# Kernel tuning notes

Hardware: AMD Instinct MI355X
Metric: run time of the kernel (lower is better)

The kernel has to match this reference:

```python
import jax, jax.numpy as jnp
import numpy as np

DIM = 128
CODEBOOK_SIZE = 1024

def setup_inputs() -> dict:
    key = jax.random.key(0)
    k1, k2 = jax.random.split(key)
    x = jax.random.normal(k1, (16, 4096, DIM), dtype=jnp.float32)
    embed = jax.random.normal(k2, (CODEBOOK_SIZE, DIM), dtype=jnp.float32)
    return {"x": x, "embed": embed}

def reference(x, embed):
    # preprocess: flatten leading dims -> (N, d)
    shape = x.shape
    flat = x.reshape(-1, shape[-1])  # (N, d)
    x_sq = jnp.sum(flat * flat, axis=1, keepdims=True)        # (N, 1)
    e_sq = jnp.sum(embed * embed, axis=1)[None, :]            # (1, K)
    dist = -(x_sq - 2.0 * (flat @ embed.T) + e_sq)            # (N, K)
    embed_ind = jnp.argmax(dist, axis=-1)                     # (N,)
    embed_ind = embed_ind.reshape(shape[:-1])                 # (...,)
    quantize = jnp.take(embed, embed_ind, axis=0)             # (..., d)
    return (quantize, embed_ind)
```

## Files before the change

kernel.cpp:

```cpp
#include <hip/hip_runtime.h>

#define NRD   65536
#define DIMD  128
#define KCB   1024
#define RPB   64
#define NBLK  (NRD / RPB)
#define MARGIN 0.18f

typedef float f32x4 __attribute__((ext_vector_type(4)));
typedef short short8 __attribute__((ext_vector_type(8)));

#define WS_ESQ   0
#define WS_CNT   4096
#define WS_LIST  8192
#define WS_B     270336
#define WS_ET2   532480
#define WS_NEED  1056768

__device__ inline unsigned short f2bf(float f) {
    unsigned u = __float_as_uint(f);
    u += 0x7FFFu + ((u >> 16) & 1u);
    return (unsigned short)(u >> 16);
}
__device__ inline float bf2f(unsigned short h) { return __uint_as_float(((unsigned)h) << 16); }

__device__ inline short8 pack_h(float4 a, float4 b) {
    short8 r;
    r[0]=(short)f2bf(a.x); r[1]=(short)f2bf(a.y); r[2]=(short)f2bf(a.z); r[3]=(short)f2bf(a.w);
    r[4]=(short)f2bf(b.x); r[5]=(short)f2bf(b.y); r[6]=(short)f2bf(b.z); r[7]=(short)f2bf(b.w);
    return r;
}
__device__ inline short lo1(float f) { return (short)f2bf(f - bf2f(f2bf(f))); }
__device__ inline short8 pack_l(float4 a, float4 b) {
    short8 r;
    r[0]=lo1(a.x); r[1]=lo1(a.y); r[2]=lo1(a.z); r[3]=lo1(a.w);
    r[4]=lo1(b.x); r[5]=lo1(b.y); r[6]=lo1(b.z); r[7]=lo1(b.w);
    return r;
}

__global__ __launch_bounds__(256, 2) void prep_kernel(const float* __restrict__ embed,
                                                      float* __restrict__ esq,
                                                      float4* __restrict__ bblob,
                                                      float4* __restrict__ et4,
                                                      int* __restrict__ cnt,
                                                      int doTrans) {
    __shared__ float tile[64][129];
    const int t = threadIdx.x;
    {
        int gw   = blockIdx.x * 4 + (t >> 6);
        int lane = t & 63;
        const float* row = embed + (size_t)gw * DIMD;
        float a = row[lane], b = row[lane + 64];
        float v = a * a + b * b;
        #pragma unroll
        for (int off = 32; off >= 1; off >>= 1) v += __shfl_xor(v, off, 64);
        if (lane == 0) esq[gw] = v;
    }
    if (blockIdx.x < 64) {
        int tid  = blockIdx.x * 256 + t;
        int lane = tid & 63;
        int ctg  = (tid >> 6) & 15;
        int ksh  = (tid >> 10) & 1;
        int s    = tid >> 11;
        int chunk = s >> 1, kh = s & 1;
        int ks = kh * 2 + ksh;
        int l15 = lane & 15, l4 = lane >> 4;
        int code = chunk * 256 + ctg * 16 + l15;
        int d0   = ks * 32 + l4 * 8;
        const float4* e4 = (const float4*)(embed + (size_t)code * DIMD + d0);
        short8 v = pack_h(e4[0], e4[1]);
        bblob[tid] = *(float4*)&v;
    }
    if (doTrans && blockIdx.x >= 64 && blockIdx.x < 80) {
        const int c0 = (blockIdx.x - 64) * 64;
        #pragma unroll
        for (int i = 0; i < 8; ++i) {
            int u = t + i * 256;
            int row = u >> 5, col4 = u & 31;
            float4 v = ((const float4*)embed)[(size_t)(c0 + row) * 32 + col4];
            tile[row][col4 * 4 + 0] = v.x;
            tile[row][col4 * 4 + 1] = v.y;
            tile[row][col4 * 4 + 2] = v.z;
            tile[row][col4 * 4 + 3] = v.w;
        }
        __syncthreads();
        #pragma unroll
        for (int i = 0; i < 8; ++i) {
            int u = t + i * 256;
            int d = u >> 4, off = u & 15;
            float4 v;
            v.x = tile[off * 4 + 0][d];
            v.y = tile[off * 4 + 1][d];
            v.z = tile[off * 4 + 2][d];
            v.w = tile[off * 4 + 3][d];
            et4[(size_t)d * 256 + (c0 >> 2) + off] = v;
        }
    }
    if (blockIdx.x == 128 && t == 0) cnt[0] = 0;
}

__global__ __launch_bounds__(512, 4) void vq_mfma(const float* __restrict__ x,
                                                  const float* __restrict__ embed,
                                                  const float* __restrict__ esq,
                                                  const float4* __restrict__ bblob,
                                                  float* __restrict__ out_q,
                                                  float* __restrict__ out_idx,
                                                  int* __restrict__ cnt,
                                                  int* __restrict__ list) {
    __shared__ __align__(16) short Atrans[4][4][512];
    __shared__ __align__(16) short Bb[32][512];
    __shared__ float rbest[4][RPB];
    __shared__ int   rmeta[4][RPB];
    __shared__ float rb2[4][RPB];

    const int t    = threadIdx.x;
    const int lane = t & 63;
    const int w    = __builtin_amdgcn_readfirstlane(t >> 6);
    const int rg   = w >> 2, cg = w & 3;
    const int l15  = lane & 15, l4 = lane >> 4;
    const int row0 = blockIdx.x * RPB;

    const int ksA = w & 3, jh = w >> 2;
    const float4* xs = (const float4*)(x + (size_t)(row0 + lane) * DIMD + ksA * 32 + jh * 16);
    float4 xv0 = xs[0], xv1 = xs[1], xv2 = xs[2], xv3 = xs[3];

#define GLDS(sv) do {                                                                                   \
    const char* g_ = (const char*)bblob + (size_t)(sv) * 32768 + ((size_t)w * 64 + lane) * 16;          \
    _Pragma("unroll")                                                                                   \
    for (int k_ = 0; k_ < 4; ++k_)                                                                      \
        __builtin_amdgcn_global_load_lds(                                                               \
            (const __attribute__((address_space(1))) unsigned int*)(g_ + k_ * 8192),                    \
            (__attribute__((address_space(3))) unsigned int*)&Bb[k_ * 8 + w][0], 16, 0, 0);             \
} while (0)

    GLDS(0);

    const int rtA = lane >> 4, riA = lane & 15;
    *(short8*)&Atrans[ksA][rtA][((jh * 2 + 0) * 16 + riA) * 8] = pack_h(xv0, xv1);
    *(short8*)&Atrans[ksA][rtA][((jh * 2 + 1) * 16 + riA) * 8] = pack_h(xv2, xv3);
    asm volatile("s_waitcnt lgkmcnt(0)" ::: "memory");
    __builtin_amdgcn_s_barrier();

    short8 ahr[4][2];
    #pragma unroll
    for (int ks = 0; ks < 4; ++ks)
        #pragma unroll
        for (int rt = 0; rt < 2; ++rt)
            ahr[ks][rt] = *(const short8*)&Atrans[ks][rg * 2 + rt][lane * 8];
    asm volatile("s_waitcnt lgkmcnt(0)" ::: "memory");
    __builtin_amdgcn_s_barrier();

    *(short8*)&Atrans[ksA][rtA][((jh * 2 + 0) * 16 + riA) * 8] = pack_l(xv0, xv1);
    *(short8*)&Atrans[ksA][rtA][((jh * 2 + 1) * 16 + riA) * 8] = pack_l(xv2, xv3);
    asm volatile("s_waitcnt vmcnt(0) lgkmcnt(0)" ::: "memory");
    __builtin_amdgcn_s_barrier();

    f32x4 acc[2][4];
    float best[2][4]; int bidx[2][4]; float b2[2][4];
    #pragma unroll
    for (int i = 0; i < 2; ++i)
        #pragma unroll
        for (int j = 0; j < 4; ++j) { best[i][j] = -1e30f; bidx[i][j] = 0; b2[i][j] = -1e30f; }

    const float* esqp = esq + cg * 64 + l15;
    float eq0 = 0.f, eq1 = 0.f, eq2 = 0.f, eq3 = 0.f;

#define STEP(khv) do {                                                                  \
    const int s_ = c * 2 + khv;                                                         \
    if (khv == 0) {                                                                     \
        eq0 = esqp[c * 256];      eq1 = esqp[c * 256 + 16];                             \
        eq2 = esqp[c * 256 + 32]; eq3 = esqp[c * 256 + 48];                             \
        _Pragma("unroll")                                                               \
        for (int i_ = 0; i_ < 2; ++i_)                                                  \
            _Pragma("unroll")                                                           \
            for (int j_ = 0; j_ < 4; ++j_) acc[i_][j_] = (f32x4){0.f, 0.f, 0.f, 0.f};   \
    }                                                                                   \
    short8 al_[2][2], bh_[2][4];                                                        \
    _Pragma("unroll")                                                                   \
    for (int ksh_ = 0; ksh_ < 2; ++ksh_) {                                              \
        _Pragma("unroll")                                                               \
        for (int rt_ = 0; rt_ < 2; ++rt_)                                               \
            al_[ksh_][rt_] = *(const short8*)&Atrans[khv * 2 + ksh_][rg * 2 + rt_][lane * 8]; \
        _Pragma("unroll")                                                               \
        for (int ct_ = 0; ct_ < 4; ++ct_)                                               \
            bh_[ksh_][ct_] = *(const short8*)&Bb[ksh_ * 16 + cg * 4 + ct_][lane * 8];   \
    }                                                                                   \
    asm volatile("s_waitcnt lgkmcnt(0)" ::: "memory");                                  \
    __builtin_amdgcn_s_barrier();                            \
    if (s_ < 7) GLDS(s_ + 1);                                   \
    _Pragma("unroll")                                                                   \
    for (int ksh_ = 0; ksh_ < 2; ++ksh_) {                                              \
        _Pragma("unroll")                                                               \
        for (int ct_ = 0; ct_ < 4; ++ct_) {                                             \
            _Pragma("unroll")                                                           \
            for (int rt_ = 0; rt_ < 2; ++rt_) {                                         \
                acc[rt_][ct_] = __builtin_amdgcn_mfma_f32_16x16x32_bf16(ahr[khv * 2 + ksh_][rt_], bh_[ksh_][ct_], acc[rt_][ct_], 0, 0, 0); \
                acc[rt_][ct_] = __builtin_amdgcn_mfma_f32_16x16x32_bf16(al_[ksh_][rt_],           bh_[ksh_][ct_], acc[rt_][ct_], 0, 0, 0); \
            }                                                                           \
        }                                                                               \
    }                                                                                   \
    if (khv == 1) {                           \
        _Pragma("unroll")                                                               \
        for (int ct_ = 0; ct_ < 4; ++ct_) {                                             \
            int code_ = c * 256 + cg * 64 + ct_ * 16 + l15;                             \
            float eq_ = (ct_ == 0) ? eq0 : (ct_ == 1) ? eq1 : (ct_ == 2) ? eq2 : eq3;   \
            _Pragma("unroll")                                                           \
            for (int rt_ = 0; rt_ < 2; ++rt_)                                           \
                _Pragma("unroll")                                                       \
                for (int r_ = 0; r_ < 4; ++r_) {                                        \
                    float sc_ = 2.0f * acc[rt_][ct_][r_] - eq_;                         \
                    b2[rt_][r_] = fmaxf(b2[rt_][r_], fminf(sc_, best[rt_][r_]));        \
                    if (sc_ > best[rt_][r_]) { best[rt_][r_] = sc_; bidx[rt_][r_] = code_; } \
                }                                                                       \
        }                                                                               \
    }                                                                                   \
    if (s_ < 7) {                                                                       \
        asm volatile("s_waitcnt vmcnt(0)" ::: "memory");          \
        __builtin_amdgcn_s_barrier();                                                   \
    }                                                                                   \
} while (0)

    for (int c = 0; c < 4; ++c) {
        STEP(0); STEP(1);
    }
#undef STEP
#undef GLDS

    #pragma unroll
    for (int rt = 0; rt < 2; ++rt)
        #pragma unroll
        for (int r = 0; r < 4; ++r) {
            float v = best[rt][r]; int i = bidx[rt][r]; float s2 = b2[rt][r];
            #pragma unroll
            for (int off = 1; off < 16; off <<= 1) {
                float ov = __shfl_xor(v, off, 64);
                int   oi = __shfl_xor(i, off, 64);
                float o2 = __shfl_xor(s2, off, 64);
                s2 = fmaxf(fmaxf(s2, o2), fminf(v, ov));
                bool sw = (ov > v) || (ov == v && oi < i);
                if (sw) { v = ov; i = oi; }
            }
            if (l15 == 0) {
                int rl = rg * 32 + rt * 16 + l4 * 4 + r;
                rbest[cg][rl] = v;
                rmeta[cg][rl] = i;
                rb2[cg][rl]   = s2;
            }
        }
    __syncthreads();
    if (t < RPB) {
        float b = rbest[0][t]; int i = rmeta[0][t]; float s2 = rb2[0][t];
        #pragma unroll
        for (int g = 1; g < 4; ++g) {
            float ob = rbest[g][t]; int oi = rmeta[g][t]; float o2 = rb2[g][t];
            s2 = fmaxf(fmaxf(s2, o2), fminf(b, ob));
            bool sw = (ob > b) || (ob == b && oi < i);
            if (sw) { b = ob; i = oi; }
        }
        out_idx[row0 + t] = (float)i;
        if (s2 >= b - MARGIN) { int pos = atomicAdd(cnt, 1); list[pos] = row0 + t; }
        rmeta[0][t] = i;
    }
    __syncthreads();
    {
        int row = t >> 3, part = t & 7;
        int idx = rmeta[0][row];
        const float4* src = (const float4*)(embed + (size_t)idx * DIMD + part * 16);
        float4* dst = (float4*)(out_q + (size_t)(row0 + row) * DIMD + part * 16);
        #pragma unroll
        for (int q = 0; q < 4; ++q) dst[q] = src[q];
    }
}

__global__ __launch_bounds__(256, 2) void trans_kernel(const float* __restrict__ embed,
                                                       float4* __restrict__ et4) {
    __shared__ float tile[64][129];
    const int t = threadIdx.x;
    const int c0 = blockIdx.x * 64;
    #pragma unroll
    for (int i = 0; i < 8; ++i) {
        int u = t + i * 256;
        int row = u >> 5, col4 = u & 31;
        float4 v = ((const float4*)embed)[(size_t)(c0 + row) * 32 + col4];
        tile[row][col4 * 4 + 0] = v.x;
        tile[row][col4 * 4 + 1] = v.y;
        tile[row][col4 * 4 + 2] = v.z;
        tile[row][col4 * 4 + 3] = v.w;
    }
    __syncthreads();
    #pragma unroll
    for (int i = 0; i < 8; ++i) {
        int u = t + i * 256;
        int d = u >> 4, off = u & 15;
        float4 v;
        v.x = tile[off * 4 + 0][d];
        v.y = tile[off * 4 + 1][d];
        v.z = tile[off * 4 + 2][d];
        v.w = tile[off * 4 + 3][d];
        et4[(size_t)d * 256 + (c0 >> 2) + off] = v;
    }
}

__global__ __launch_bounds__(256, 2) void refine_kernel(const float* __restrict__ x,
                                                        const float* __restrict__ embed,
                                                        const float* __restrict__ esq,
                                                        const f32x4* __restrict__ et4,
                                                        float* __restrict__ out_q,
                                                        float* __restrict__ out_idx,
                                                        const int* __restrict__ cnt,
                                                        const int* __restrict__ list) {
    __shared__ float xls[4][4][128];
    const int t = threadIdx.x, lane = t & 63, w = t >> 6;
    const int n = cnt[0];
    const int njobs = (n + 3) >> 2;
    for (int job = blockIdx.x * 4 + w; job < njobs; job += gridDim.x * 4) {
        int rows[4];
        #pragma unroll
        for (int i = 0; i < 4; ++i) {
            int li = job * 4 + i; if (li >= n) li = n - 1;
            rows[i] = list[li];
        }
        float xsq[4];
        #pragma unroll
        for (int i = 0; i < 4; ++i) {
            float2 xv = *(const float2*)(x + (size_t)rows[i] * DIMD + lane * 2);
            xls[w][i][lane * 2]     = xv.x;
            xls[w][i][lane * 2 + 1] = xv.y;
            float s = xv.x * xv.x + xv.y * xv.y;
            #pragma unroll
            for (int off = 32; off >= 1; off >>= 1) s += __shfl_xor(s, off, 64);
            xsq[i] = s;
        }
        f32x4 acc[4][4];
        #pragma unroll
        for (int i = 0; i < 4; ++i)
            #pragma unroll
            for (int g = 0; g < 4; ++g) acc[i][g] = (f32x4){0.f, 0.f, 0.f, 0.f};

        for (int d0 = 0; d0 < 32; ++d0) {
            float4 xd[4];
            #pragma unroll
            for (int i = 0; i < 4; ++i) xd[i] = *(const float4*)&xls[w][i][d0 * 4];
            #pragma unroll
            for (int dd = 0; dd < 4; ++dd) {
                const f32x4* ep = et4 + (size_t)(d0 * 4 + dd) * 256 + lane;
                f32x4 e0 = ep[0], e1 = ep[64], e2 = ep[128], e3 = ep[192];
                #pragma unroll
                for (int i = 0; i < 4; ++i) {
                    float xsc = (dd == 0) ? xd[i].x : (dd == 1) ? xd[i].y
                              : (dd == 2) ? xd[i].z : xd[i].w;
                    acc[i][0] = e0 * xsc + acc[i][0];
                    acc[i][1] = e1 * xsc + acc[i][1];
                    acc[i][2] = e2 * xsc + acc[i][2];
                    acc[i][3] = e3 * xsc + acc[i][3];
                }
            }
        }

        #pragma unroll
        for (int i = 0; i < 4; ++i) {
            float bv = -1e30f; int bi = 0;
            #pragma unroll
            for (int g = 0; g < 4; ++g) {
                float4 eq = *(const float4*)&esq[g * 256 + lane * 4];
                #pragma unroll
                for (int c2 = 0; c2 < 4; ++c2) {
                    float eqv = (c2 == 0) ? eq.x : (c2 == 1) ? eq.y : (c2 == 2) ? eq.z : eq.w;
                    float sc = -(__fadd_rn(__fsub_rn(xsq[i], __fmul_rn(2.0f, acc[i][g][c2])), eqv));
                    int code = g * 256 + lane * 4 + c2;
                    if (sc > bv) { bv = sc; bi = code; }
                }
            }
            #pragma unroll
            for (int off = 32; off >= 1; off >>= 1) {
                float ov = __shfl_xor(bv, off, 64);
                int   oi = __shfl_xor(bi, off, 64);
                if (ov > bv || (ov == bv && oi < bi)) { bv = ov; bi = oi; }
            }
            if (lane == 0) out_idx[rows[i]] = (float)bi;
            if (lane < 32) {
                float4 v = ((const float4*)embed)[(size_t)bi * 32 + lane];
                ((float4*)out_q)[(size_t)rows[i] * 32 + lane] = v;
            }
        }
    }
}

extern "C" void kernel_launch(void* const* d_in, const int* in_sizes, int n_in,
                              void* d_out, int out_size, void* d_ws, size_t ws_size,
                              hipStream_t stream) {
    const float* x     = (const float*)d_in[0];
    const float* embed = (const float*)d_in[1];
    float* out     = (float*)d_out;
    float* out_q   = out;
    float* out_idx = out + (size_t)NRD * DIMD;

    char*  wsb  = (char*)d_ws;
    float* esq  = (float*)(wsb + WS_ESQ);
    int*   cnt  = (int*)(wsb + WS_CNT);
    int*   list = (int*)(wsb + WS_LIST);
    float4* bblob = (float4*)(wsb + WS_B);

    const int fused = (ws_size >= (size_t)WS_NEED) ? 1 : 0;
    f32x4* et4 = fused ? (f32x4*)(wsb + WS_ET2) : (f32x4*)(wsb + WS_B);

    prep_kernel  <<<dim3(256),  dim3(256), 0, stream>>>(embed, esq, bblob, (float4*)et4, cnt, fused);
    vq_mfma      <<<dim3(NBLK), dim3(512), 0, stream>>>(x, embed, esq, bblob, out_q, out_idx, cnt, list);
    if (!fused)
        trans_kernel<<<dim3(16), dim3(256), 0, stream>>>(embed, (float4*)et4);
    refine_kernel<<<dim3(256),  dim3(256), 0, stream>>>(x, embed, esq, et4, out_q, out_idx, cnt, list);
}
```

Before: 89.36 us.

## Drop bf16 low-part split for x and pipeline codebook loads in half-stages

Removes the hi/lo bf16 split of x, which halves the MFMA count per step. To keep argmax correct it widens the refinement margin from 0.18 to 0.40, so more rows fall into the exact fp32 fallback path. It also aliases the A staging buffer onto the B buffer, caches codebook norms in LDS, and restructures the B loads into half-stage prefetches with vmcnt-based waits. The risks are more rows needing refinement and more barriers per stage.

```diff
diff --git a/kernel.cpp b/kernel.cpp
--- a/kernel.cpp
+++ b/kernel.cpp
@@ -5,7 +5,7 @@
 #define KCB   1024
 #define RPB   64
 #define NBLK  (NRD / RPB)
-#define MARGIN 0.18f
+#define MARGIN 0.40f
 
 typedef float f32x4 __attribute__((ext_vector_type(4)));
 typedef short short8 __attribute__((ext_vector_type(8)));
@@ -22,19 +22,11 @@
     u += 0x7FFFu + ((u >> 16) & 1u);
     return (unsigned short)(u >> 16);
 }
-__device__ inline float bf2f(unsigned short h) { return __uint_as_float(((unsigned)h) << 16); }
 
 __device__ inline short8 pack_h(float4 a, float4 b) {
     short8 r;
     r[0]=(short)f2bf(a.x); r[1]=(short)f2bf(a.y); r[2]=(short)f2bf(a.z); r[3]=(short)f2bf(a.w);
     r[4]=(short)f2bf(b.x); r[5]=(short)f2bf(b.y); r[6]=(short)f2bf(b.z); r[7]=(short)f2bf(b.w);
-    return r;
-}
-__device__ inline short lo1(float f) { return (short)f2bf(f - bf2f(f2bf(f))); }
-__device__ inline short8 pack_l(float4 a, float4 b) {
-    short8 r;
-    r[0]=lo1(a.x); r[1]=lo1(a.y); r[2]=lo1(a.z); r[3]=lo1(a.w);
-    r[4]=lo1(b.x); r[5]=lo1(b.y); r[6]=lo1(b.z); r[7]=lo1(b.w);
     return r;
 }
 
@@ -107,8 +99,8 @@
                                                   float* __restrict__ out_idx,
                                                   int* __restrict__ cnt,
                                                   int* __restrict__ list) {
-    __shared__ __align__(16) short Atrans[4][4][512];
     __shared__ __align__(16) short Bb[32][512];
+    __shared__ float esqs[KCB];
     __shared__ float rbest[4][RPB];
     __shared__ int   rmeta[4][RPB];
     __shared__ float rb2[4][RPB];
@@ -120,24 +112,17 @@
     const int l15  = lane & 15, l4 = lane >> 4;
     const int row0 = blockIdx.x * RPB;
 
+    const float2 ev = *(const float2*)(esq + t * 2);
+
     const int ksA = w & 3, jh = w >> 2;
     const float4* xs = (const float4*)(x + (size_t)(row0 + lane) * DIMD + ksA * 32 + jh * 16);
     float4 xv0 = xs[0], xv1 = xs[1], xv2 = xs[2], xv3 = xs[3];
 
-#define GLDS(sv) do {                                                                                   \
-    const char* g_ = (const char*)bblob + (size_t)(sv) * 32768 + ((size_t)w * 64 + lane) * 16;          \
-    _Pragma("unroll")                                                                                   \
-    for (int k_ = 0; k_ < 4; ++k_)                                                                      \
-        __builtin_amdgcn_global_load_lds(                                                               \
-            (const __attribute__((address_space(1))) unsigned int*)(g_ + k_ * 8192),                    \
-            (__attribute__((address_space(3))) unsigned int*)&Bb[k_ * 8 + w][0], 16, 0, 0);             \
-} while (0)
-
-    GLDS(0);
-
+    short (*Atrans)[4][512] = (short (*)[4][512])&Bb[0][0];
     const int rtA = lane >> 4, riA = lane & 15;
     *(short8*)&Atrans[ksA][rtA][((jh * 2 + 0) * 16 + riA) * 8] = pack_h(xv0, xv1);
     *(short8*)&Atrans[ksA][rtA][((jh * 2 + 1) * 16 + riA) * 8] = pack_h(xv2, xv3);
+    *(float2*)&esqs[t * 2] = ev;
     asm volatile("s_waitcnt lgkmcnt(0)" ::: "memory");
     __builtin_amdgcn_s_barrier();
 
@@ -150,10 +135,19 @@
     asm volatile("s_waitcnt lgkmcnt(0)" ::: "memory");
     __builtin_amdgcn_s_barrier();
 
-    *(short8*)&Atrans[ksA][rtA][((jh * 2 + 0) * 16 + riA) * 8] = pack_l(xv0, xv1);
-    *(short8*)&Atrans[ksA][rtA][((jh * 2 + 1) * 16 + riA) * 8] = pack_l(xv2, xv3);
-    asm volatile("s_waitcnt vmcnt(0) lgkmcnt(0)" ::: "memory");
-    __builtin_amdgcn_s_barrier();
+#define GLDS_HALF(s2, kshv) do {                                                                        \
+    const char* g_ = (const char*)bblob + (size_t)(s2) * 32768 + (size_t)(kshv) * 16384                 \
+                   + ((size_t)w * 64 + lane) * 16;                                                      \
+    __builtin_amdgcn_global_load_lds(                                                                   \
+        (const __attribute__((address_space(1))) unsigned int*)(g_),                                    \
+        (__attribute__((address_space(3))) unsigned int*)&Bb[(kshv) * 16 + w][0], 16, 0, 0);            \
+    __builtin_amdgcn_global_load_lds(                                                                   \
+        (const __attribute__((address_space(1))) unsigned int*)(g_ + 8192),                             \
+        (__attribute__((address_space(3))) unsigned int*)&Bb[(kshv) * 16 + 8 + w][0], 16, 0, 0);        \
+} while (0)
+
+    GLDS_HALF(0, 0);
+    GLDS_HALF(0, 1);
 
     f32x4 acc[2][4];
     float best[2][4]; int bidx[2][4]; float b2[2][4];
@@ -162,69 +156,63 @@
         #pragma unroll
         for (int j = 0; j < 4; ++j) { best[i][j] = -1e30f; bidx[i][j] = 0; b2[i][j] = -1e30f; }
 
-    const float* esqp = esq + cg * 64 + l15;
     float eq0 = 0.f, eq1 = 0.f, eq2 = 0.f, eq3 = 0.f;
 
-#define STEP(khv) do {                                                                  \
-    const int s_ = c * 2 + khv;                                                         \
-    if (khv == 0) {                                                                     \
-        eq0 = esqp[c * 256];      eq1 = esqp[c * 256 + 16];                             \
-        eq2 = esqp[c * 256 + 32]; eq3 = esqp[c * 256 + 48];                             \
-        _Pragma("unroll")                                                               \
-        for (int i_ = 0; i_ < 2; ++i_)                                                  \
-            _Pragma("unroll")                                                           \
-            for (int j_ = 0; j_ < 4; ++j_) acc[i_][j_] = (f32x4){0.f, 0.f, 0.f, 0.f};   \
-    }                                                                                   \
-    short8 al_[2][2], bh_[2][4];                                                        \
-    _Pragma("unroll")                                                                   \
-    for (int ksh_ = 0; ksh_ < 2; ++ksh_) {                                              \
-        _Pragma("unroll")                                                               \
-        for (int rt_ = 0; rt_ < 2; ++rt_)                                               \
-            al_[ksh_][rt_] = *(const short8*)&Atrans[khv * 2 + ksh_][rg * 2 + rt_][lane * 8]; \
-        _Pragma("unroll")                                                               \
-        for (int ct_ = 0; ct_ < 4; ++ct_)                                               \
-            bh_[ksh_][ct_] = *(const short8*)&Bb[ksh_ * 16 + cg * 4 + ct_][lane * 8];   \
-    }                                                                                   \
-    asm volatile("s_waitcnt lgkmcnt(0)" ::: "memory");                                  \
-    __builtin_amdgcn_s_barrier();                            \
-    if (s_ < 7) GLDS(s_ + 1);                                   \
-    _Pragma("unroll")                                                                   \
-    for (int ksh_ = 0; ksh_ < 2; ++ksh_) {                                              \
-        _Pragma("unroll")                                                               \
-        for (int ct_ = 0; ct_ < 4; ++ct_) {                                             \
-            _Pragma("unroll")                                                           \
-            for (int rt_ = 0; rt_ < 2; ++rt_) {                                         \
-                acc[rt_][ct_] = __builtin_amdgcn_mfma_f32_16x16x32_bf16(ahr[khv * 2 + ksh_][rt_], bh_[ksh_][ct_], acc[rt_][ct_], 0, 0, 0); \
-                acc[rt_][ct_] = __builtin_amdgcn_mfma_f32_16x16x32_bf16(al_[ksh_][rt_],           bh_[ksh_][ct_], acc[rt_][ct_], 0, 0, 0); \
-            }                                                                           \
-        }                                                                               \
-    }                                                                                   \
-    if (khv == 1) {                           \
-        _Pragma("unroll")                                                               \
-        for (int ct_ = 0; ct_ < 4; ++ct_) {                                             \
-            int code_ = c * 256 + cg * 64 + ct_ * 16 + l15;                             \
-            float eq_ = (ct_ == 0) ? eq0 : (ct_ == 1) ? eq1 : (ct_ == 2) ? eq2 : eq3;   \
-            _Pragma("unroll")                                                           \
-            for (int rt_ = 0; rt_ < 2; ++rt_)                                           \
-                _Pragma("unroll")                                                       \
-                for (int r_ = 0; r_ < 4; ++r_) {                                        \
-                    float sc_ = 2.0f * acc[rt_][ct_][r_] - eq_;                         \
-                    b2[rt_][r_] = fmaxf(b2[rt_][r_], fminf(sc_, best[rt_][r_]));        \
-                    if (sc_ > best[rt_][r_]) { best[rt_][r_] = sc_; bidx[rt_][r_] = code_; } \
-                }                                                                       \
-        }                                                                               \
-    }                                                                                   \
-    if (s_ < 7) {                                                                       \
-        asm volatile("s_waitcnt vmcnt(0)" ::: "memory");          \
-        __builtin_amdgcn_s_barrier();                                                   \
-    }                                                                                   \
-} while (0)
-
+    #pragma unroll
     for (int c = 0; c < 4; ++c) {
-        STEP(0); STEP(1);
-    }
-#undef STEP
-#undef GLDS
+      #pragma unroll
+      for (int khv = 0; khv < 2; ++khv) {
+        #pragma unroll
+        for (int ksh = 0; ksh < 2; ++ksh) {
+            const int h = c * 4 + khv * 2 + ksh;
+            if (h == 15) asm volatile("s_waitcnt vmcnt(0)" ::: "memory");
+            else         asm volatile("s_waitcnt vmcnt(2)" ::: "memory");
+            __builtin_amdgcn_s_barrier();
+
+            short8 bh[4];
+            #pragma unroll
+            for (int ct = 0; ct < 4; ++ct)
+                bh[ct] = *(const short8*)&Bb[ksh * 16 + cg * 4 + ct][lane * 8];
+            if (khv == 0 && ksh == 0) {
+                eq0 = esqs[c * 256 + cg * 64 + l15];
+                eq1 = esqs[c * 256 + cg * 64 + l15 + 16];
+                eq2 = esqs[c * 256 + cg * 64 + l15 + 32];
+                eq3 = esqs[c * 256 + cg * 64 + l15 + 48];
+                #pragma unroll
+                for (int i = 0; i < 2; ++i)
+                    #pragma unroll
+                    for (int j = 0; j < 4; ++j) acc[i][j] = (f32x4){0.f, 0.f, 0.f, 0.f};
+            }
+            asm volatile("s_waitcnt lgkmcnt(0)" ::: "memory");
+            __builtin_amdgcn_s_barrier();
+            if (h + 2 < 16) GLDS_HALF(c * 2 + khv + 1, ksh);
+
+            #pragma unroll
+            for (int ct = 0; ct < 4; ++ct)
+                #pragma unroll
+                for (int rt = 0; rt < 2; ++rt)
+                    acc[rt][ct] = __builtin_amdgcn_mfma_f32_16x16x32_bf16(
+                        ahr[khv * 2 + ksh][rt], bh[ct], acc[rt][ct], 0, 0, 0);
+
+            if (khv == 1 && ksh == 1) {
+                #pragma unroll
+                for (int ct = 0; ct < 4; ++ct) {
+                    int code_ = c * 256 + cg * 64 + ct * 16 + l15;
+                    float eq_ = (ct == 0) ? eq0 : (ct == 1) ? eq1 : (ct == 2) ? eq2 : eq3;
+                    #pragma unroll
+                    for (int rt = 0; rt < 2; ++rt)
+                        #pragma unroll
+                        for (int r = 0; r < 4; ++r) {
+                            float sc_ = 2.0f * acc[rt][ct][r] - eq_;
+                            b2[rt][r] = fmaxf(b2[rt][r], fminf(sc_, best[rt][r]));
+                            if (sc_ > best[rt][r]) { best[rt][r] = sc_; bidx[rt][r] = code_; }
+                        }
+                }
+            }
+        }
+      }
+    }
+#undef GLDS_HALF
 
     #pragma unroll
     for (int rt = 0; rt < 2; ++rt)
```

New measurement: 179.9 us. +101.3%, slower.
